# Kernel tuning notes

Measured on AMD Instinct MI355X. Metric: run time of the kernel, lower is better.

The kernel has to match this reference:

```python
import jax, jax.numpy as jnp
import numpy as np

# ---- static problem dims (mirror the Triton kernel's constexprs) ----
NUM_SEQS = 2
LQ = 1024            # query tokens per sequence (uniform varlen instance)
HIST = 1024          # cached-prefix length per sequence
LK = LQ + HIST       # total kv length per sequence
NUM_HEADS = 32
NUM_KV_HEADS = 8
HEAD_DIM = 128
BLOCK_SIZE = 64
MAX_NUM_BLOCKS = LK // BLOCK_SIZE          # 32 logical blocks per sequence
TOTAL_BLOCKS = NUM_SEQS * MAX_NUM_BLOCKS   # physical blocks in the cache
NEG = -1e10                                # matches kernel's -10000000000.0


def setup_inputs() -> dict:
    key = jax.random.key(0)
    k1, k2, k3, k4 = jax.random.split(key, 4)
    q = jax.random.normal(k1, (NUM_SEQS * LQ, NUM_HEADS, HEAD_DIM), jnp.float32)
    k_cache = jax.random.normal(k2, (TOTAL_BLOCKS, BLOCK_SIZE, NUM_KV_HEADS, HEAD_DIM), jnp.float32)
    v_cache = jax.random.normal(k3, (TOTAL_BLOCKS, BLOCK_SIZE, NUM_KV_HEADS, HEAD_DIM), jnp.float32)
    cu_seqlens_q = (jnp.arange(NUM_SEQS + 1, dtype=jnp.int32) * LQ)
    cu_seqlens_k = (jnp.arange(NUM_SEQS + 1, dtype=jnp.int32) * LK)
    # scattered physical block layout: a random permutation -> irregular gather
    block_tables = jax.random.permutation(k4, TOTAL_BLOCKS).astype(jnp.int32).reshape(NUM_SEQS, MAX_NUM_BLOCKS)
    return dict(q=q, k_cache=k_cache, v_cache=v_cache,
                cu_seqlens_q=cu_seqlens_q, cu_seqlens_k=cu_seqlens_k,
                block_tables=block_tables)


def _paged_prefill_attention(q, k_cache, v_cache, cu_seqlens_q, cu_seqlens_k, block_tables):
    scale = 1.0 / np.sqrt(HEAD_DIM)
    seq_len_q = cu_seqlens_q[1:] - cu_seqlens_q[:-1]            # [S]
    seq_len_k = cu_seqlens_k[1:] - cu_seqlens_k[:-1]            # [S]
    history_len = seq_len_k - seq_len_q                          # [S]

    # uniform varlen instance: flat [total_q, H, D] -> [S, LQ, H, D]
    qr = q.reshape(NUM_SEQS, LQ, NUM_HEADS, HEAD_DIM)
    group = NUM_HEADS // NUM_KV_HEADS
    # [S, LQ, KVH, G, D] so head h maps to kv head h // group (kernel's kv_head_idx)
    q5 = qr.reshape(NUM_SEQS, LQ, NUM_KV_HEADS, group, HEAD_DIM) * scale

    # block-table gather: logical kv layout per sequence
    safe_tables = jnp.maximum(block_tables, 0)
    k = k_cache[safe_tables].reshape(NUM_SEQS, LK, NUM_KV_HEADS, HEAD_DIM)
    v = v_cache[safe_tables].reshape(NUM_SEQS, LK, NUM_KV_HEADS, HEAD_DIM)

    # scores [S, KVH, G, LQ, LK]
    scores = jnp.einsum('sqhgd,skhd->shgqk', q5, k)

    pos_q = jnp.arange(LQ, dtype=jnp.int32)[None, :] + history_len[:, None]   # [S, LQ] absolute positions
    pos_k = jnp.arange(LK, dtype=jnp.int32)                                   # [LK]
    valid_k = (pos_k[None, :] < seq_len_k[:, None]) & \
              jnp.repeat(block_tables >= 0, BLOCK_SIZE, axis=1)               # [S, LK]
    causal = pos_q[:, :, None] >= pos_k[None, None, :]                        # [S, LQ, LK]
    mask = causal & valid_k[:, None, :]
    scores = jnp.where(mask[:, None, None, :, :], scores, NEG)

    p = jax.nn.softmax(scores, axis=-1)  # online-softmax in kernel == exact softmax
    out = jnp.einsum('shgqk,skhd->sqhgd', p, v)
    return out.reshape(NUM_SEQS * LQ, NUM_HEADS, HEAD_DIM)


def reference(q, k_cache, v_cache, cu_seqlens_q, cu_seqlens_k, block_tables):
    return _paged_prefill_attention(q, k_cache, v_cache, cu_seqlens_q, cu_seqlens_k, block_tables)
```

## Files before the change

### kernel.cpp

```cpp
#include <hip/hip_runtime.h>
#include <hip/hip_bf16.h>

#define NS_    2
#define LQ_    1024
#define HIST_  1024
#define LK_    2048
#define NH_    32
#define NKVH_  8
#define HD_    128
#define BS_    64
#define BM_    128
#define MAXB_  32

typedef __attribute__((ext_vector_type(8))) short short8;
typedef __attribute__((ext_vector_type(4))) float f32x4;

#define VSTR 72

static __device__ __forceinline__ unsigned short f2bf(float x) {
    __hip_bfloat16 h = __float2bfloat16(x);
    return *(unsigned short*)&h;
}

static __device__ __forceinline__ void cp16(const void* g, void* l) {
    __builtin_amdgcn_global_load_lds(
        (const __attribute__((address_space(1))) void*)g,
        (__attribute__((address_space(3))) void*)l, 16, 0, 0);
}

template<int CTRL>
static __device__ __forceinline__ float dppmax(float x) {
    int y = __builtin_amdgcn_update_dpp(0, __float_as_int(x), CTRL, 0xf, 0xf, true);
    return fmaxf(x, __int_as_float(y));
}

__global__ __launch_bounds__(256)
void prep_kv(const float* __restrict__ kc, const float* __restrict__ vc,
             const int* __restrict__ bt,
             unsigned short* __restrict__ Kb, unsigned short* __restrict__ Vb)
{
    __shared__ __align__(16) unsigned short Vt[HD_ * VSTR];
    const int tid = threadIdx.x;
    const int gid = blockIdx.x;
    const int seq = gid >> 8;
    const int kvh = (gid >> 5) & 7;
    const int blk = gid & 31;
    const int ph  = bt[seq * MAXB_ + blk];
    const size_t src = ((size_t)ph * BS_ * NKVH_ + kvh) * HD_;
    const int grp = seq * NKVH_ + kvh;
    const int t8 = tid >> 5, q32 = tid & 31;

    float4 kr[8], vr[8];
#pragma unroll
    for (int p = 0; p < 8; ++p)
        kr[p] = *(const float4*)(kc + src + (size_t)(p * 8 + t8) * (NKVH_ * HD_) + q32 * 4);
#pragma unroll
    for (int j = 0; j < 8; ++j)
        vr[j] = *(const float4*)(vc + src + (size_t)(t8 * 8 + j) * (NKVH_ * HD_) + q32 * 4);

#pragma unroll
    for (int p = 0; p < 8; ++p) {
        unsigned short u[4] = {f2bf(kr[p].x), f2bf(kr[p].y), f2bf(kr[p].z), f2bf(kr[p].w)};
        *(uint2*)(Kb + ((size_t)grp * LK_ + blk * BS_ + p * 8 + t8) * HD_ + q32 * 4) = *(const uint2*)u;
    }
#pragma unroll
    for (int w2 = 0; w2 < 4; ++w2) {
        unsigned short row[8];
#pragma unroll
        for (int j = 0; j < 8; ++j) {
            float f = (w2 == 0) ? vr[j].x : (w2 == 1) ? vr[j].y : (w2 == 2) ? vr[j].z : vr[j].w;
            row[j] = f2bf(f);
        }
        *(short8*)&Vt[(q32 * 4 + w2) * VSTR + t8 * 8] = *(const short8*)row;
    }
    __syncthreads();
#pragma unroll
    for (int u = 0; u < 4; ++u) {
        const int c  = tid + 256 * u;
        const int d  = c >> 3, ch = c & 7;
        uint4 x = *(const uint4*)&Vt[d * VSTR + ch * 8];
        *(uint4*)(Vb + ((size_t)grp * HD_ + d) * LK_ + blk * BS_ + ch * 8) = x;
    }
}

template<bool PREP>
__global__ __launch_bounds__(512, 4)
void paged_attn(const float* __restrict__ q,
                const unsigned short* __restrict__ Kb,
                const unsigned short* __restrict__ Vb,
                const float* __restrict__ kc,
                const float* __restrict__ vc,
                const int* __restrict__ bt,
                float* __restrict__ out)
{
    __shared__ __align__(16) unsigned short Ksh[2][BS_ * HD_];
    __shared__ __align__(16) unsigned short Vsh[2][HD_ * BS_];
    __shared__ __align__(16) unsigned short Psh[BM_ * BS_];

    const int tid  = threadIdx.x;
    const int w    = tid >> 6;
    const int lane = tid & 63;
    const int n    = lane & 15;
    const int q4   = lane >> 4;

    const int gid  = blockIdx.x;
    const int kvh  = gid & 7;
    const int slot = gid >> 3;
    const int seq  = slot >> 5;
    const int sub  = slot & 31;
    const int e    = sub & 1;
    const int t3   = (sub >> 1) & 7;
    const int hp   = sub >> 4;
    const int head = kvh * 4 + hp * 2 + e;
    const int m0   = (e ? (7 - t3) : t3) * BM_;
    const int r0   = m0 + w * 16;
    const int grp  = seq * NKVH_ + kvh;

    const float SC = 0.08838834764831845f * 1.4426950408889634f;
    short8 qf[4];
    {
        const size_t base = ((size_t)((seq * LQ_ + r0 + n) * NH_ + head)) * HD_;
#pragma unroll
        for (int c = 0; c < 4; ++c) {
            float4 a = *(const float4*)(q + base + c * 32 + q4 * 8);
            float4 b = *(const float4*)(q + base + c * 32 + q4 * 8 + 4);
            unsigned short u[8] = {f2bf(a.x * SC), f2bf(a.y * SC), f2bf(a.z * SC), f2bf(a.w * SC),
                                   f2bf(b.x * SC), f2bf(b.y * SC), f2bf(b.z * SC), f2bf(b.w * SC)};
            qf[c] = *(const short8*)u;
        }
    }

    f32x4 acc[8];
    f32x4 lf = (f32x4){0.f, 0.f, 0.f, 0.f};
    float mrow[4];
#pragma unroll
    for (int dt = 0; dt < 8; ++dt) acc[dt] = (f32x4){0.f, 0.f, 0.f, 0.f};
#pragma unroll
    for (int r = 0; r < 4; ++r) mrow[r] = -1e30f;

    const int nb = (HIST_ + m0 + BM_ - 1) / BS_ + 1;
    const unsigned short* kSrc = Kb + (size_t)grp * LK_ * HD_;
    const unsigned short* vSrc = Vb + (size_t)grp * HD_ * LK_;

    auto issue = [&](int b, int buf) {
#pragma unroll
        for (int j = 0; j < 2; ++j) {
            const int row = w * 8 + j * 4 + (lane >> 4);
            const int c8  = (lane & 15) ^ (row & 15);
            cp16(kSrc + ((size_t)b * BS_ + row) * HD_ + c8 * 8, &Ksh[buf][(w * 8 + j * 4) * HD_]);
        }
#pragma unroll
        for (int j = 0; j < 2; ++j) {
            const int d  = w * 16 + j * 8 + (lane >> 3);
            const int c8 = (lane & 7) ^ (d & 7);
            cp16(vSrc + (size_t)d * LK_ + b * BS_ + c8 * 8, &Vsh[buf][(w * 16 + j * 8) * BS_]);
        }
    };

    if constexpr (PREP) issue(0, 0);
    short8 ones;
#pragma unroll
    for (int j = 0; j < 8; ++j) ones[j] = (short)0x3F80;

    for (int b = 0; b < nb; ++b) {
        const int cur = PREP ? (b & 1) : 0;
        __syncthreads();
        if constexpr (PREP) {
            if (b + 1 < nb) issue(b + 1, 1 ^ cur);
        } else {
            const int ph = bt[seq * MAXB_ + b];
            const size_t src = ((size_t)ph * BS_ * NKVH_ + kvh) * HD_;
#pragma unroll
            for (int j = 0; j < 2; ++j) {
                const int row = w * 8 + j * 4 + (lane >> 4);
                const int c8  = (lane & 15) ^ (row & 15);
                float4 a = *(const float4*)(kc + src + (size_t)row * (NKVH_ * HD_) + c8 * 8);
                float4 b2 = *(const float4*)(kc + src + (size_t)row * (NKVH_ * HD_) + c8 * 8 + 4);
                unsigned short u[8] = {f2bf(a.x), f2bf(a.y), f2bf(a.z), f2bf(a.w),
                                       f2bf(b2.x), f2bf(b2.y), f2bf(b2.z), f2bf(b2.w)};
                *(short8*)&Ksh[0][row * HD_ + (lane & 15) * 8] = *(const short8*)u;
            }
#pragma unroll
            for (int j = 0; j < 2; ++j) {
                const int d  = w * 16 + j * 8 + (lane >> 3);
                const int c8 = (lane & 7) ^ (d & 7);
                unsigned short u[8];
#pragma unroll
                for (int i2 = 0; i2 < 8; ++i2)
                    u[i2] = f2bf(vc[src + (size_t)(c8 * 8 + i2) * (NKVH_ * HD_) + d]);
                *(short8*)&Vsh[0][d * BS_ + (lane & 7) * 8] = *(const short8*)u;
            }
            __syncthreads();
        }

        if (64 * b <= HIST_ + r0 + 15) {
            f32x4 s[4];
#pragma unroll
            for (int kt = 0; kt < 4; ++kt) s[kt] = (f32x4){0.f, 0.f, 0.f, 0.f};
            __builtin_amdgcn_s_setprio(1);
#pragma unroll
            for (int kt = 0; kt < 4; ++kt) {
#pragma unroll
                for (int c = 0; c < 4; ++c) {
                    short8 kf = *(const short8*)&Ksh[cur][(kt * 16 + n) * HD_ + (((c * 4 + q4) ^ n) << 3)];
                    s[kt] = __builtin_amdgcn_mfma_f32_16x16x32_bf16(qf[c], kf, s[kt], 0, 0, 0);
                }
            }
            __builtin_amdgcn_s_setprio(0);

            const bool needMask = (64 * b + 63 > HIST_ + r0);
            float mx[4], al[4];
#pragma unroll
            for (int r = 0; r < 4; ++r) mx[r] = -1e30f;
#pragma unroll
            for (int kt = 0; kt < 4; ++kt) {
#pragma unroll
                for (int r = 0; r < 4; ++r) {
                    float t = s[kt][r];
                    if (needMask) {
                        const int key = b * 64 + kt * 16 + n;
                        const int row = r0 + q4 * 4 + r;
                        if (key > HIST_ + row) t = -1e30f;
                    }
                    s[kt][r] = t;
                    mx[r] = fmaxf(mx[r], t);
                }
            }
#pragma unroll
            for (int r = 0; r < 4; ++r) {
                mx[r] = dppmax<0xB1>(mx[r]);
                mx[r] = dppmax<0x4E>(mx[r]);
                mx[r] = dppmax<0x124>(mx[r]);
                mx[r] = dppmax<0x128>(mx[r]);
                const float mn = fmaxf(mrow[r], mx[r]);
                al[r] = __builtin_amdgcn_exp2f(mrow[r] - mn);
                mrow[r] = mn;
            }
            const int rbase = w * 16 + q4 * 4;
#pragma unroll
            for (int kt = 0; kt < 4; ++kt) {
                const int cb = kt * 2 + (n >> 3);
                const int ci = n & 7;
#pragma unroll
                for (int r = 0; r < 4; ++r) {
                    const int row = rbase + r;
                    const float p = __builtin_amdgcn_exp2f(s[kt][r] - mrow[r]);
                    Psh[row * BS_ + ((cb ^ (row & 7)) << 3) + ci] = f2bf(p);
                }
            }
            if (__any(al[0] != 1.f || al[1] != 1.f || al[2] != 1.f || al[3] != 1.f)) {
#pragma unroll
                for (int dt = 0; dt < 8; ++dt)
#pragma unroll
                    for (int r = 0; r < 4; ++r) acc[dt][r] *= al[r];
#pragma unroll
                for (int r = 0; r < 4; ++r) lf[r] *= al[r];
            }
            __builtin_amdgcn_s_setprio(1);
#pragma unroll
            for (int ks = 0; ks < 2; ++ks) {
                short8 pa = *(const short8*)&Psh[(w * 16 + n) * BS_ + (((ks * 4 + q4) ^ (n & 7)) << 3)];
                lf = __builtin_amdgcn_mfma_f32_16x16x32_bf16(pa, ones, lf, 0, 0, 0);
#pragma unroll
                for (int dt = 0; dt < 8; ++dt) {
                    short8 vf = *(const short8*)&Vsh[cur][(dt * 16 + n) * BS_ + (((ks * 4 + q4) ^ (n & 7)) << 3)];
                    acc[dt] = __builtin_amdgcn_mfma_f32_16x16x32_bf16(pa, vf, acc[dt], 0, 0, 0);
                }
            }
            __builtin_amdgcn_s_setprio(0);
        }
    }

    {
        float rl[4];
#pragma unroll
        for (int r = 0; r < 4; ++r) rl[r] = 1.0f / lf[r];
#pragma unroll
        for (int dt = 0; dt < 8; ++dt)
#pragma unroll
            for (int r = 0; r < 4; ++r) {
                const int row = r0 + q4 * 4 + r;
                out[((size_t)((seq * LQ_ + row) * NH_ + head)) * HD_ + dt * 16 + n] = acc[dt][r] * rl[r];
            }
    }
}

extern "C" void kernel_launch(void* const* d_in, const int* in_sizes, int n_in,
                              void* d_out, int out_size, void* d_ws, size_t ws_size,
                              hipStream_t stream) {
    const float* q  = (const float*)d_in[0];
    const float* kc = (const float*)d_in[1];
    const float* vc = (const float*)d_in[2];
    const int*   bt = (const int*)d_in[5];
    float*      out = (float*)d_out;
    (void)in_sizes; (void)n_in; (void)out_size;

    const size_t kb_elems = (size_t)NS_ * NKVH_ * LK_ * HD_;
    const size_t need = kb_elems * 2 * sizeof(unsigned short);
    if (ws_size >= need) {
        unsigned short* Kb = (unsigned short*)d_ws;
        unsigned short* Vb = Kb + kb_elems;
        prep_kv<<<512, 256, 0, stream>>>(kc, vc, bt, Kb, Vb);
        paged_attn<true><<<512, 512, 0, stream>>>(q, Kb, Vb, kc, vc, bt, out);
    } else {
        paged_attn<false><<<512, 512, 0, stream>>>(q, nullptr, nullptr, kc, vc, bt, out);
    }
}
```

Baseline: 202.6 us.

## Load V fragments directly from global into registers instead of LDS

Removes the V shared-memory double buffer and its async copies. Each wave now loads its V MFMA operands straight from global memory (pre-converted bf16 V for the PREP path, fp32 cache with conversion otherwise) into registers, split into two halves issued around the softmax and the first PV MFMA batch. This cuts LDS traffic and footprint, which could raise occupancy. In exchange every wave redundantly fetches the same V tile from global/L2, and there is no cross-block prefetch for V, so load latency may be exposed.

```diff
diff --git a/kernel.cpp b/kernel.cpp
--- a/kernel.cpp
+++ b/kernel.cpp
@@ -94,7 +94,6 @@
                 float* __restrict__ out)
 {
     __shared__ __align__(16) unsigned short Ksh[2][BS_ * HD_];
-    __shared__ __align__(16) unsigned short Vsh[2][HD_ * BS_];
     __shared__ __align__(16) unsigned short Psh[BM_ * BS_];
 
     const int tid  = threadIdx.x;
@@ -149,12 +148,6 @@
             const int c8  = (lane & 15) ^ (row & 15);
             cp16(kSrc + ((size_t)b * BS_ + row) * HD_ + c8 * 8, &Ksh[buf][(w * 8 + j * 4) * HD_]);
         }
-#pragma unroll
-        for (int j = 0; j < 2; ++j) {
-            const int d  = w * 16 + j * 8 + (lane >> 3);
-            const int c8 = (lane & 7) ^ (d & 7);
-            cp16(vSrc + (size_t)d * LK_ + b * BS_ + c8 * 8, &Vsh[buf][(w * 16 + j * 8) * BS_]);
-        }
     };
 
     if constexpr (PREP) issue(0, 0);
@@ -179,16 +172,6 @@
                 unsigned short u[8] = {f2bf(a.x), f2bf(a.y), f2bf(a.z), f2bf(a.w),
                                        f2bf(b2.x), f2bf(b2.y), f2bf(b2.z), f2bf(b2.w)};
                 *(short8*)&Ksh[0][row * HD_ + (lane & 15) * 8] = *(const short8*)u;
-            }
-#pragma unroll
-            for (int j = 0; j < 2; ++j) {
-                const int d  = w * 16 + j * 8 + (lane >> 3);
-                const int c8 = (lane & 7) ^ (d & 7);
-                unsigned short u[8];
-#pragma unroll
-                for (int i2 = 0; i2 < 8; ++i2)
-                    u[i2] = f2bf(vc[src + (size_t)(c8 * 8 + i2) * (NKVH_ * HD_) + d]);
-                *(short8*)&Vsh[0][d * BS_ + (lane & 7) * 8] = *(const short8*)u;
             }
             __syncthreads();
         }
@@ -236,6 +219,14 @@
                 al[r] = __builtin_amdgcn_exp2f(mrow[r] - mn);
                 mrow[r] = mn;
             }
+
+            short8 v0[8];
+            if constexpr (PREP) {
+#pragma unroll
+                for (int dt = 0; dt < 8; ++dt)
+                    v0[dt] = *(const short8*)(vSrc + (size_t)(dt * 16 + n) * LK_ + b * BS_ + q4 * 8);
+            }
+
             const int rbase = w * 16 + q4 * 4;
 #pragma unroll
             for (int kt = 0; kt < 4; ++kt) {
@@ -256,18 +247,55 @@
 #pragma unroll
                 for (int r = 0; r < 4; ++r) lf[r] *= al[r];
             }
-            __builtin_amdgcn_s_setprio(1);
-#pragma unroll
-            for (int ks = 0; ks < 2; ++ks) {
-                short8 pa = *(const short8*)&Psh[(w * 16 + n) * BS_ + (((ks * 4 + q4) ^ (n & 7)) << 3)];
+
+            if constexpr (!PREP) {
+                const int ph = bt[seq * MAXB_ + b];
+                const size_t srcV = ((size_t)ph * BS_ * NKVH_ + kvh) * HD_;
+#pragma unroll
+                for (int dt = 0; dt < 8; ++dt) {
+                    unsigned short u[8];
+#pragma unroll
+                    for (int i2 = 0; i2 < 8; ++i2)
+                        u[i2] = f2bf(vc[srcV + (size_t)(q4 * 8 + i2) * (NKVH_ * HD_) + dt * 16 + n]);
+                    v0[dt] = *(const short8*)u;
+                }
+            }
+
+            {
+                short8 pa = *(const short8*)&Psh[(w * 16 + n) * BS_ + ((q4 ^ (n & 7)) << 3)];
+                __builtin_amdgcn_s_setprio(1);
                 lf = __builtin_amdgcn_mfma_f32_16x16x32_bf16(pa, ones, lf, 0, 0, 0);
 #pragma unroll
-                for (int dt = 0; dt < 8; ++dt) {
-                    short8 vf = *(const short8*)&Vsh[cur][(dt * 16 + n) * BS_ + (((ks * 4 + q4) ^ (n & 7)) << 3)];
-                    acc[dt] = __builtin_amdgcn_mfma_f32_16x16x32_bf16(pa, vf, acc[dt], 0, 0, 0);
-                }
-            }
-            __builtin_amdgcn_s_setprio(0);
+                for (int dt = 0; dt < 8; ++dt)
+                    acc[dt] = __builtin_amdgcn_mfma_f32_16x16x32_bf16(pa, v0[dt], acc[dt], 0, 0, 0);
+                __builtin_amdgcn_s_setprio(0);
+            }
+            {
+                short8 v1[8];
+                if constexpr (PREP) {
+#pragma unroll
+                    for (int dt = 0; dt < 8; ++dt)
+                        v1[dt] = *(const short8*)(vSrc + (size_t)(dt * 16 + n) * LK_ + b * BS_ + 32 + q4 * 8);
+                } else {
+                    const int ph = bt[seq * MAXB_ + b];
+                    const size_t srcV = ((size_t)ph * BS_ * NKVH_ + kvh) * HD_;
+#pragma unroll
+                    for (int dt = 0; dt < 8; ++dt) {
+                        unsigned short u[8];
+#pragma unroll
+                        for (int i2 = 0; i2 < 8; ++i2)
+                            u[i2] = f2bf(vc[srcV + (size_t)(32 + q4 * 8 + i2) * (NKVH_ * HD_) + dt * 16 + n]);
+                        v1[dt] = *(const short8*)u;
+                    }
+                }
+                short8 pb = *(const short8*)&Psh[(w * 16 + n) * BS_ + (((4 + q4) ^ (n & 7)) << 3)];
+                __builtin_amdgcn_s_setprio(1);
+                lf = __builtin_amdgcn_mfma_f32_16x16x32_bf16(pb, ones, lf, 0, 0, 0);
+#pragma unroll
+                for (int dt = 0; dt < 8; ++dt)
+                    acc[dt] = __builtin_amdgcn_mfma_f32_16x16x32_bf16(pb, v1[dt], acc[dt], 0, 0, 0);
+                __builtin_amdgcn_s_setprio(0);
+            }
         }
     }
 
```

Result: slower. 553.2 us (+173.0%).
